# Performance work log

Hardware: AMD Instinct MI355X
Metric: run time of the kernel (lower is better)

## Reference

```python
import jax, jax.numpy as jnp
import numpy as np
import math

N, IN_DIM, Z, H, OUT, K = 16384, 64, 128, 1, 3, 16


def setup_inputs() -> dict:
    key = jax.random.key(0)
    ks = jax.random.split(key, 16)

    def lin(k, din, dout):
        kw, kb = jax.random.split(k)
        W = jax.random.normal(kw, (din, dout), jnp.float32) / math.sqrt(din)
        b = jax.random.normal(kb, (dout,), jnp.float32) * 0.01
        return W, b

    x = jax.random.normal(ks[0], (N, IN_DIM), jnp.float32)
    t = jnp.zeros((1,), jnp.float32)
    # layer dims: (in, heads*out) per TransformerConv
    dims = [(IN_DIM, Z * H), (Z * H, (Z // H) * H), (Z * H, (OUT // H) * H)]
    params = {}
    i = 1
    for li, (din, dout) in enumerate(dims, 1):
        for nm in ("q", "k", "v", "s"):
            W, b = lin(ks[i], din, dout)
            i += 1
            params[f"W{nm}{li}"] = W
            params[f"b{nm}{li}"] = b
    return {"t": t, "x": x, **params}


def knn_edge_index(coo, k):
    # kNN graph on 3-D coords (loop=False): edges neighbor(src) -> center(dst)
    n = coo.shape[0]
    sq = jnp.sum(coo * coo, axis=-1)
    d = sq[:, None] + sq[None, :] - 2.0 * (coo @ coo.T)  # [N, N] sq. distances
    d = d.at[jnp.arange(n), jnp.arange(n)].set(jnp.inf)  # exclude self-loops
    _, idx = jax.lax.top_k(-d, k)  # [N, K] nearest neighbor indices
    src = idx.reshape(-1)
    dst = jnp.repeat(jnp.arange(n), k)
    return src, dst


def tconv(x, src, dst, Wq, bq, Wk, bk, Wv, bv, Ws, bs, heads):
    # PyG TransformerConv (concat=True, root_weight=True, no edge_attr)
    n = x.shape[0]
    dout = Wq.shape[1]
    c = dout // heads
    q = (x @ Wq + bq).reshape(n, heads, c)
    kk = (x @ Wk + bk).reshape(n, heads, c)
    v = (x @ Wv + bv).reshape(n, heads, c)
    alpha = jnp.sum(q[dst] * kk[src], axis=-1) / math.sqrt(c)  # [E, H]
    amax = jax.ops.segment_max(alpha, dst, num_segments=n)
    ex = jnp.exp(alpha - amax[dst])
    denom = jax.ops.segment_sum(ex, dst, num_segments=n)
    w = ex / denom[dst]  # softmax over incoming edges per node
    msg = w[:, :, None] * v[src]  # [E, H, C]
    out = jax.ops.segment_sum(msg, dst, num_segments=n).reshape(n, dout)
    return out + x @ Ws + bs  # root/skip connection


def reference(t, x,
              Wq1, bq1, Wk1, bk1, Wv1, bv1, Ws1, bs1,
              Wq2, bq2, Wk2, bk2, Wv2, bv2, Ws2, bs2,
              Wq3, bq3, Wk3, bk3, Wv3, bv3, Ws3, bs3):
    src, dst = knn_edge_index(x[:, :3], K)  # built under no_grad in original
    h = jnp.tanh(tconv(x, src, dst, Wq1, bq1, Wk1, bk1, Wv1, bv1, Ws1, bs1, H))
    h = jnp.tanh(tconv(h, src, dst, Wq2, bq2, Wk2, bk2, Wv2, bv2, Ws2, bs2, H) + h)
    drift_coo = tconv(h, src, dst, Wq3, bq3, Wk3, bk3, Wv3, bv3, Ws3, bs3, H)
    return drift_coo
```

## Files before the change

### kernel.cpp

```cpp
#include <hip/hip_runtime.h>
#include <math.h>

#define NN 16384
#define QPW 2
#define CAP 128
#define WM 64
#define KTOP 17

typedef unsigned long long u64;

__global__ __launch_bounds__(256) void pack_coords(const float* __restrict__ x,
                                                   float4* __restrict__ coo) {
  int i = blockIdx.x * 256 + threadIdx.x;
  float a = x[i * 64 + 0];
  float b = x[i * 64 + 1];
  float c = x[i * 64 + 2];
  coo[i] = make_float4(a, b, c, a * a + b * b + c * c);
}

__device__ __forceinline__ int mbcnt64(u64 mask) {
  return __builtin_amdgcn_mbcnt_hi(
      (unsigned)(mask >> 32),
      __builtin_amdgcn_mbcnt_lo((unsigned)mask, 0));
}

__device__ __forceinline__ unsigned fmap(float d) {
  unsigned ub = __float_as_uint(d);
  return ub ^ ((unsigned)((int)ub >> 31) | 0x80000000u);
}

__device__ __forceinline__ float unfmap(unsigned ub) {
  unsigned fb = (ub & 0x80000000u) ? (ub ^ 0x80000000u) : ~ub;
  return __uint_as_float(fb);
}

__device__ __forceinline__ u64 u64min(u64 a, u64 b) { return a < b ? a : b; }
__device__ __forceinline__ u64 u64max(u64 a, u64 b) { return a > b ? a : b; }

__device__ __forceinline__ void sort128(u64& r0, u64& r1, int lane) {
#pragma unroll
  for (int k = 2; k <= 128; k <<= 1) {
    if (k == 128) {
      u64 lo = u64min(r0, r1);
      r1 = u64max(r0, r1);
      r0 = lo;
    }
#pragma unroll
    for (int jj = (k == 128 ? 32 : (k >> 1)); jj >= 1; jj >>= 1) {
      const bool up = (lane & jj) == 0;
      const bool asc0 = (lane & k) == 0;
      const bool asc1 = ((lane | 64) & k) == 0;
      u64 o0 = __shfl_xor(r0, jj);
      u64 o1 = __shfl_xor(r1, jj);
      r0 = (up == asc0) ? u64min(r0, o0) : u64max(r0, o0);
      r1 = (up == asc1) ? u64min(r1, o1) : u64max(r1, o1);
    }
  }
}

__device__ __forceinline__ void radix_shrink(u64* buf, int& cnt, float& th,
                                             int lane) {
  const u64 k0 = (lane < cnt) ? buf[lane] : ~0ull;
  const u64 k1 = (lane + 64 < cnt) ? buf[lane + 64] : ~0ull;
  const unsigned d0 = (unsigned)(k0 >> 32);
  const unsigned d1 = (unsigned)(k1 >> 32);
  unsigned p = 0u;
#pragma unroll
  for (int b = 31; b >= 0; --b) {
    const unsigned c = p | (1u << b);
    const u64 b0 = __ballot(d0 < c);
    const u64 b1 = __ballot(d1 < c);
    const int n = __popcll(b0) + __popcll(b1);
    if (n < KTOP) p = c;
  }
  const bool v0 = d0 <= p;
  const bool v1 = d1 <= p;
  const u64 m0 = __ballot(v0);
  const u64 m1 = __ballot(v1);
  const int base = __popcll(m0);
  if (v0) buf[mbcnt64(m0)] = k0;
  if (v1) buf[base + mbcnt64(m1)] = k1;
  cnt = base + __popcll(m1);
  th = unfmap(p);
}

__global__ __launch_bounds__(256) void knn_kernel(const float4* __restrict__ coo,
                                                  int* __restrict__ src) {
  __shared__ u64 bufs[4][QPW][CAP];
  const int lane = threadIdx.x & 63;
  const int wid = threadIdx.x >> 6;
  const int node0 = blockIdx.x * (4 * QPW) + wid * QPW;

  float nx[QPW], ny[QPW], nz[QPW], sq[QPW], th[QPW];
  int cnt[QPW];
#pragma unroll
  for (int q = 0; q < QPW; ++q) {
    const float4 me = coo[node0 + q];
    nx[q] = -2.0f * me.x;
    ny[q] = -2.0f * me.y;
    nz[q] = -2.0f * me.z;
    sq[q] = me.w;
    th[q] = __builtin_inff();
    cnt[q] = 0;
  }

  float4 cur = coo[lane];
  float4 nxt = coo[64 + lane];

#pragma unroll 2
  for (int step = 0; step < NN / 64; ++step) {
    float4 fut = make_float4(0.f, 0.f, 0.f, 0.f);
    if (step + 2 < NN / 64) fut = coo[(step + 2) * 64 + lane];
    const int j = step * 64 + lane;

    float dd[QPW];
#pragma unroll
    for (int q = 0; q < QPW; ++q) {
      float a = fmaf(nz[q], cur.z, cur.w);
      a = fmaf(ny[q], cur.y, a);
      a = fmaf(nx[q], cur.x, a);
      dd[q] = sq[q] + a;
    }
    u64 mk[QPW];
#pragma unroll
    for (int q = 0; q < QPW; ++q) mk[q] = __ballot(dd[q] <= th[q]);

    if (mk[0] | mk[1]) {
#pragma unroll
      for (int q = 0; q < QPW; ++q) {
        if (mk[q]) {
          if (dd[q] <= th[q]) {
            const int pos = cnt[q] + mbcnt64(mk[q]);
            bufs[wid][q][pos] = ((u64)fmap(dd[q]) << 32) | (unsigned)j;
          }
          cnt[q] += __popcll(mk[q]);
        }
      }
      if ((cnt[0] >= WM) || (cnt[1] >= WM)) {
#pragma unroll
        for (int q = 0; q < QPW; ++q)
          if (cnt[q] >= WM) radix_shrink(bufs[wid][q], cnt[q], th[q], lane);
      }
    }
    cur = nxt;
    nxt = fut;
  }

#pragma unroll 1
  for (int q = 0; q < QPW; ++q) {
    u64 r0 = (lane < cnt[q]) ? bufs[wid][q][lane] : ~0ull;
    u64 r1 = (lane + 64 < cnt[q]) ? bufs[wid][q][lane + 64] : ~0ull;
    sort128(r0, r1, lane);
    const int idx = (int)(r0 & 0xFFFFFFFFull);
    const u64 selfm = __ballot((lane < KTOP) && (idx == node0 + q));
    const int s = selfm ? (__ffsll((long long)selfm) - 1) : 99;
    const int outrank = lane - (lane > s ? 1 : 0);
    if (lane < KTOP && lane != s && outrank < 16)
      src[(node0 + q) * 16 + outrank] = idx;
  }
}

template <int KD>
__global__ __launch_bounds__(256) void gemm_qkvs(
    const float* __restrict__ X, const float* __restrict__ W0,
    const float* __restrict__ W1, const float* __restrict__ W2,
    const float* __restrict__ W3, const float* __restrict__ B0,
    const float* __restrict__ B1, const float* __restrict__ B2,
    const float* __restrict__ B3, float* __restrict__ out) {
  __shared__ float As[64][68];
  __shared__ float Bs[64][64];
  const int brow = blockIdx.x * 64;
  const int by = blockIdx.y;
  const int wi = by >> 1;
  const float* W = wi == 0 ? W0 : wi == 1 ? W1 : wi == 2 ? W2 : W3;
  const float* bias = wi == 0 ? B0 : wi == 1 ? B1 : wi == 2 ? B2 : B3;
  const int cbase = (by & 1) * 64;
  const int tx = threadIdx.x & 15;
  const int ty = threadIdx.x >> 4;

  float acc[4][4] = {};
  for (int k0 = 0; k0 < KD; k0 += 64) {
    __syncthreads();
#pragma unroll
    for (int i = 0; i < 4; ++i) {
      const int flat = threadIdx.x * 4 + i * 1024;
      const int r = flat >> 6, kk = flat & 63;
      *(float4*)&As[r][kk] = *(const float4*)&X[(brow + r) * KD + k0 + kk];
    }
#pragma unroll
    for (int i = 0; i < 4; ++i) {
      const int flat = threadIdx.x * 4 + i * 1024;
      const int kk = flat >> 6, c = flat & 63;
      *(float4*)&Bs[kk][c] = *(const float4*)&W[(k0 + kk) * 128 + cbase + c];
    }
    __syncthreads();
#pragma unroll 8
    for (int k = 0; k < 64; ++k) {
      const float4 b = *(const float4*)&Bs[k][tx * 4];
      const float bv[4] = {b.x, b.y, b.z, b.w};
      float av[4];
#pragma unroll
      for (int i = 0; i < 4; ++i) av[i] = As[ty * 4 + i][k];
#pragma unroll
      for (int i = 0; i < 4; ++i)
#pragma unroll
        for (int jj = 0; jj < 4; ++jj)
          acc[i][jj] = fmaf(av[i], bv[jj], acc[i][jj]);
    }
  }
  const float4 bi = *(const float4*)&bias[cbase + tx * 4];
#pragma unroll
  for (int i = 0; i < 4; ++i) {
    const int row = brow + ty * 4 + i;
    float4 o;
    o.x = acc[i][0] + bi.x;
    o.y = acc[i][1] + bi.y;
    o.z = acc[i][2] + bi.z;
    o.w = acc[i][3] + bi.w;
    *(float4*)&out[row * 512 + wi * 128 + cbase + tx * 4] = o;
  }
}

__global__ __launch_bounds__(256) void attn_c128(
    const float* __restrict__ qkvs, const int* __restrict__ src,
    const float* __restrict__ res, float* __restrict__ hout, int do_res) {
  const int lane = threadIdx.x & 63;
  const int node = blockIdx.x * 4 + (threadIdx.x >> 6);
  const float2 q2 = ((const float2*)(qkvs + node * 512))[lane];

  int nb[16];
#pragma unroll
  for (int r = 0; r < 16; ++r) nb[r] = src[node * 16 + r];

  float alpha[16];
#pragma unroll
  for (int r = 0; r < 16; ++r) {
    const float2 k2 = ((const float2*)(qkvs + nb[r] * 512 + 128))[lane];
    float p = q2.x * k2.x + q2.y * k2.y;
#pragma unroll
    for (int o = 32; o; o >>= 1) p += __shfl_xor(p, o);
    alpha[r] = p * 0.088388347648318447f;
  }
  float m = alpha[0];
#pragma unroll
  for (int r = 1; r < 16; ++r) m = fmaxf(m, alpha[r]);
  float w[16];
  float den = 0.0f;
#pragma unroll
  for (int r = 0; r < 16; ++r) { w[r] = __expf(alpha[r] - m); den += w[r]; }
  const float inv = 1.0f / den;
  float o0 = 0.0f, o1 = 0.0f;
#pragma unroll
  for (int r = 0; r < 16; ++r) {
    const float2 v2 = ((const float2*)(qkvs + nb[r] * 512 + 256))[lane];
    const float ww = w[r] * inv;
    o0 = fmaf(ww, v2.x, o0);
    o1 = fmaf(ww, v2.y, o1);
  }
  const float2 s2 = ((const float2*)(qkvs + node * 512 + 384))[lane];
  float r0 = o0 + s2.x;
  float r1 = o1 + s2.y;
  if (do_res) {
    const float2 h2 = ((const float2*)(res + node * 128))[lane];
    r0 += h2.x;
    r1 += h2.y;
  }
  ((float2*)(hout + node * 128))[lane] = make_float2(tanhf(r0), tanhf(r1));
}

__global__ __launch_bounds__(256) void gemm_qkvs3(
    const float* __restrict__ H, const float* __restrict__ W0,
    const float* __restrict__ W1, const float* __restrict__ W2,
    const float* __restrict__ W3, const float* __restrict__ B0,
    const float* __restrict__ B1, const float* __restrict__ B2,
    const float* __restrict__ B3, float* __restrict__ out) {
  __shared__ float hs[64][132];
  __shared__ float wsh[128 * 12];
  __shared__ float bsh[12];
  const int brow = blockIdx.x * 64;
  if (threadIdx.x < 12) {
    const int mi = threadIdx.x / 3, c = threadIdx.x % 3;
    const float* Bsel = mi == 0 ? B0 : mi == 1 ? B1 : mi == 2 ? B2 : B3;
    bsh[threadIdx.x] = Bsel[c];
  }
  for (int t = threadIdx.x; t < 1536; t += 256) {
    const int k = t / 12, cc = t % 12;
    const int mi = cc / 3, c = cc % 3;
    const float* Wsel = mi == 0 ? W0 : mi == 1 ? W1 : mi == 2 ? W2 : W3;
    wsh[t] = Wsel[k * 3 + c];
  }
#pragma unroll
  for (int i = 0; i < 8; ++i) {
    const int flat = threadIdx.x * 4 + i * 1024;
    const int r = flat >> 7, kk = flat & 127;
    *(float4*)&hs[r][kk] = *(const float4*)&H[(brow + r) * 128 + kk];
  }
  __syncthreads();
  const int r = threadIdx.x >> 2;
  const int part = threadIdx.x & 3;
  float a0 = 0.0f, a1 = 0.0f, a2 = 0.0f;
#pragma unroll 4
  for (int k = 0; k < 128; ++k) {
    const float h = hs[r][k];
    a0 = fmaf(h, wsh[k * 12 + part * 3 + 0], a0);
    a1 = fmaf(h, wsh[k * 12 + part * 3 + 1], a1);
    a2 = fmaf(h, wsh[k * 12 + part * 3 + 2], a2);
  }
  const int row = brow + r;
  out[row * 12 + part * 3 + 0] = a0 + bsh[part * 3 + 0];
  out[row * 12 + part * 3 + 1] = a1 + bsh[part * 3 + 1];
  out[row * 12 + part * 3 + 2] = a2 + bsh[part * 3 + 2];
}

__global__ __launch_bounds__(256) void attn_c3(const float* __restrict__ q3,
                                               const int* __restrict__ src,
                                               float* __restrict__ out) {
  const int gid = blockIdx.x * 256 + threadIdx.x;
  const int node = gid >> 4, r = gid & 15;
  const int j = src[node * 16 + r];
  const float* qn = q3 + node * 12;
  const float* kj = q3 + j * 12 + 3;
  float alpha = (qn[0] * kj[0] + qn[1] * kj[1] + qn[2] * kj[2]) *
                0.57735026918962576f;
  float m = alpha;
#pragma unroll
  for (int o = 8; o; o >>= 1) m = fmaxf(m, __shfl_xor(m, o, 16));
  const float e = __expf(alpha - m);
  float den = e;
#pragma unroll
  for (int o = 8; o; o >>= 1) den += __shfl_xor(den, o, 16);
  const float wgt = e / den;
  const float* vj = q3 + j * 12 + 6;
  float o0 = wgt * vj[0], o1 = wgt * vj[1], o2 = wgt * vj[2];
#pragma unroll
  for (int o = 8; o; o >>= 1) {
    o0 += __shfl_xor(o0, o, 16);
    o1 += __shfl_xor(o1, o, 16);
    o2 += __shfl_xor(o2, o, 16);
  }
  if (r == 0) {
    const float* sn = q3 + node * 12 + 9;
    out[node * 3 + 0] = o0 + sn[0];
    out[node * 3 + 1] = o1 + sn[1];
    out[node * 3 + 2] = o2 + sn[2];
  }
}

extern "C" void kernel_launch(void* const* d_in, const int* in_sizes, int n_in,
                              void* d_out, int out_size, void* d_ws,
                              size_t ws_size, hipStream_t stream) {
  const float* x = (const float*)d_in[1];
  const float* Wq1 = (const float*)d_in[2];
  const float* bq1 = (const float*)d_in[3];
  const float* Wk1 = (const float*)d_in[4];
  const float* bk1 = (const float*)d_in[5];
  const float* Wv1 = (const float*)d_in[6];
  const float* bv1 = (const float*)d_in[7];
  const float* Ws1 = (const float*)d_in[8];
  const float* bs1 = (const float*)d_in[9];
  const float* Wq2 = (const float*)d_in[10];
  const float* bq2 = (const float*)d_in[11];
  const float* Wk2 = (const float*)d_in[12];
  const float* bk2 = (const float*)d_in[13];
  const float* Wv2 = (const float*)d_in[14];
  const float* bv2 = (const float*)d_in[15];
  const float* Ws2 = (const float*)d_in[16];
  const float* bs2 = (const float*)d_in[17];
  const float* Wq3 = (const float*)d_in[18];
  const float* bq3 = (const float*)d_in[19];
  const float* Wk3 = (const float*)d_in[20];
  const float* bk3 = (const float*)d_in[21];
  const float* Wv3 = (const float*)d_in[22];
  const float* bv3 = (const float*)d_in[23];
  const float* Ws3 = (const float*)d_in[24];
  const float* bs3 = (const float*)d_in[25];

  char* ws = (char*)d_ws;
  float* qkvs = (float*)(ws);
  float* h1 = (float*)(ws + (size_t)32 * 1024 * 1024);
  float* h2 = (float*)(ws + (size_t)40 * 1024 * 1024);
  int* src = (int*)(ws + (size_t)48 * 1024 * 1024);
  float4* coo = (float4*)(ws + (size_t)49 * 1024 * 1024);
  float* q3 = (float*)(ws + (size_t)49 * 1024 * 1024 + 512 * 1024);
  float* out = (float*)d_out;

  pack_coords<<<NN / 256, 256, 0, stream>>>(x, coo);
  knn_kernel<<<NN / (4 * QPW), 256, 0, stream>>>(coo, src);
  gemm_qkvs<64><<<dim3(NN / 64, 8), 256, 0, stream>>>(
      x, Wq1, Wk1, Wv1, Ws1, bq1, bk1, bv1, bs1, qkvs);
  attn_c128<<<NN / 4, 256, 0, stream>>>(qkvs, src, nullptr, h1, 0);
  gemm_qkvs<128><<<dim3(NN / 64, 8), 256, 0, stream>>>(
      h1, Wq2, Wk2, Wv2, Ws2, bq2, bk2, bv2, bs2, qkvs);
  attn_c128<<<NN / 4, 256, 0, stream>>>(qkvs, src, h1, h2, 1);
  gemm_qkvs3<<<NN / 64, 256, 0, stream>>>(h2, Wq3, Wk3, Wv3, Ws3, bq3, bk3,
                                          bv3, bs3, q3);
  attn_c3<<<NN * 16 / 256, 256, 0, stream>>>(q3, src, out);
}
```

Baseline: 362.2 us.

## Widen kNN queries per wave, transpose GEMM A tile, batch attention reductions

The kNN scan now processes four query nodes per wave instead of two, so each streamed coordinate load is reused across more queries. The QKVS GEMM stores the A tile transposed in shared memory so each k-step reads a single float4 instead of four strided scalars. The attention kernel issues all 16 key loads before interleaving the 16 butterfly reductions, and prefetches all value rows ahead of the softmax to expose memory-level parallelism. These changes raise register pressure and shared-memory footprint; the transposed A store may introduce LDS bank conflicts, and the larger QPW halves the number of waves in the kNN grid.

```diff
diff --git a/kernel.cpp b/kernel.cpp
--- a/kernel.cpp
+++ b/kernel.cpp
@@ -2,7 +2,7 @@
 #include <math.h>
 
 #define NN 16384
-#define QPW 2
+#define QPW 4
 #define CAP 128
 #define WM 64
 #define KTOP 17
@@ -125,7 +125,7 @@
 #pragma unroll
     for (int q = 0; q < QPW; ++q) mk[q] = __ballot(dd[q] <= th[q]);
 
-    if (mk[0] | mk[1]) {
+    if (mk[0] | mk[1] | mk[2] | mk[3]) {
 #pragma unroll
       for (int q = 0; q < QPW; ++q) {
         if (mk[q]) {
@@ -136,7 +136,7 @@
           cnt[q] += __popcll(mk[q]);
         }
       }
-      if ((cnt[0] >= WM) || (cnt[1] >= WM)) {
+      if ((cnt[0] >= WM) | (cnt[1] >= WM) | (cnt[2] >= WM) | (cnt[3] >= WM)) {
 #pragma unroll
         for (int q = 0; q < QPW; ++q)
           if (cnt[q] >= WM) radix_shrink(bufs[wid][q], cnt[q], th[q], lane);
@@ -185,7 +185,11 @@
     for (int i = 0; i < 4; ++i) {
       const int flat = threadIdx.x * 4 + i * 1024;
       const int r = flat >> 6, kk = flat & 63;
-      *(float4*)&As[r][kk] = *(const float4*)&X[(brow + r) * KD + k0 + kk];
+      const float4 v = *(const float4*)&X[(brow + r) * KD + k0 + kk];
+      As[kk + 0][r] = v.x;
+      As[kk + 1][r] = v.y;
+      As[kk + 2][r] = v.z;
+      As[kk + 3][r] = v.w;
     }
 #pragma unroll
     for (int i = 0; i < 4; ++i) {
@@ -196,11 +200,10 @@
     __syncthreads();
 #pragma unroll 8
     for (int k = 0; k < 64; ++k) {
+      const float4 a = *(const float4*)&As[k][ty * 4];
       const float4 b = *(const float4*)&Bs[k][tx * 4];
+      const float av[4] = {a.x, a.y, a.z, a.w};
       const float bv[4] = {b.x, b.y, b.z, b.w};
-      float av[4];
-#pragma unroll
-      for (int i = 0; i < 4; ++i) av[i] = As[ty * 4 + i][k];
 #pragma unroll
       for (int i = 0; i < 4; ++i)
 #pragma unroll
@@ -232,30 +235,40 @@
 #pragma unroll
   for (int r = 0; r < 16; ++r) nb[r] = src[node * 16 + r];
 
-  float alpha[16];
+  float p[16];
 #pragma unroll
   for (int r = 0; r < 16; ++r) {
     const float2 k2 = ((const float2*)(qkvs + nb[r] * 512 + 128))[lane];
-    float p = q2.x * k2.x + q2.y * k2.y;
-#pragma unroll
-    for (int o = 32; o; o >>= 1) p += __shfl_xor(p, o);
-    alpha[r] = p * 0.088388347648318447f;
-  }
-  float m = alpha[0];
-#pragma unroll
-  for (int r = 1; r < 16; ++r) m = fmaxf(m, alpha[r]);
+    p[r] = q2.x * k2.x + q2.y * k2.y;
+  }
+#pragma unroll
+  for (int o = 32; o; o >>= 1) {
+#pragma unroll
+    for (int r = 0; r < 16; ++r) p[r] += __shfl_xor(p[r], o);
+  }
+
+  float2 v2[16];
+#pragma unroll
+  for (int r = 0; r < 16; ++r)
+    v2[r] = ((const float2*)(qkvs + nb[r] * 512 + 256))[lane];
+
+  float m = p[0];
+#pragma unroll
+  for (int r = 1; r < 16; ++r) m = fmaxf(m, p[r]);
   float w[16];
   float den = 0.0f;
 #pragma unroll
-  for (int r = 0; r < 16; ++r) { w[r] = __expf(alpha[r] - m); den += w[r]; }
+  for (int r = 0; r < 16; ++r) {
+    w[r] = __expf((p[r] - m) * 0.088388347648318447f);
+    den += w[r];
+  }
   const float inv = 1.0f / den;
   float o0 = 0.0f, o1 = 0.0f;
 #pragma unroll
   for (int r = 0; r < 16; ++r) {
-    const float2 v2 = ((const float2*)(qkvs + nb[r] * 512 + 256))[lane];
     const float ww = w[r] * inv;
-    o0 = fmaf(ww, v2.x, o0);
-    o1 = fmaf(ww, v2.y, o1);
+    o0 = fmaf(ww, v2[r].x, o0);
+    o1 = fmaf(ww, v2[r].y, o1);
   }
   const float2 s2 = ((const float2*)(qkvs + node * 512 + 384))[lane];
   float r0 = o0 + s2.x;
```

Result: slower. 381.8 us (+5.4%).
